# Optimization experiments

Hardware: AMD Instinct MI355X
Metric: run time of the kernel (lower is better)

## Reference

```python
import jax, jax.numpy as jnp
import numpy as np

EPS = 1e-8  # torch.nn.CosineSimilarity default eps

B, N, C, H, W = 256, 5, 640, 10, 10
OC, OH, OW = 32, 5, 5  # AdaptiveAvgPool3d output (input_dim, 5, 5)


def _pool(v):
    # Adaptive avg pool over last 3 dims (C,H,W) -> (OC,OH,OW).
    # Exact block-mean since C%OC==0, H%OH==0, W%OW==0.
    lead = v.shape[:-3]
    v = v.reshape(lead + (OC, C // OC, OH, H // OH, OW, W // OW))
    return v.mean(axis=(-5, -3, -1))


def setup_inputs() -> dict:
    key = jax.random.key(0)
    x = jax.random.normal(key, (B, N, C, H, W), dtype=jnp.float32)
    return {"x": x}


def reference(x) -> jnp.ndarray:
    b, n = x.shape[0], x.shape[1]
    # proxy: pool of the sum over shots -> [B, OC*OH*OW]
    proxy = _pool(x.sum(axis=1)).reshape(b, -1)
    # per-shot pooled features -> [B, N, OC*OH*OW]
    feats = _pool(x).reshape(b, n, -1)
    # cosine similarity (torch formula: dot / max(||a||*||b||, eps))
    dot = jnp.einsum('bnd,bd->bn', feats, proxy)
    na = jnp.linalg.norm(feats, axis=-1)          # [B, N]
    nb = jnp.linalg.norm(proxy, axis=-1)[:, None]  # [B, 1]
    sim = dot / jnp.maximum(na * nb, EPS)          # [B, N]
    # weighted sum of raw shot features -> [B, C, H, W]
    out = jnp.einsum('bn,bnchw->bchw', sim, x)
    return out
```

## Files before the change

kernel.cpp:

```cpp
#include <hip/hip_runtime.h>

#define BB 256
#define NN 5
#define CC_ 640
#define HH 10
#define WW 10
#define CHW 64000
#define DD 800
#define EPSF 1e-8f

__global__ __launch_bounds__(256) void k_pool(const float* __restrict__ x,
                                              float* __restrict__ feats) {
    const int bn = blockIdx.x;
    const float2* __restrict__ xp =
        reinterpret_cast<const float2*>(x + (size_t)bn * CHW);
    float* __restrict__ fp = feats + (size_t)bn * DD;
    for (int d = threadIdx.x; d < DD; d += 256) {
        const int oc  = d / 25;
        const int rem = d - oc * 25;
        const int oh  = rem / 5;
        const int ow  = rem - oh * 5;
        int base = oc * 20 * 50 + oh * 10 + ow;
        float s = 0.f;
        #pragma unroll
        for (int cc = 0; cc < 20; ++cc) {
            float2 a = xp[base + cc * 50];
            float2 b = xp[base + cc * 50 + 5];
            s += (a.x + a.y) + (b.x + b.y);
        }
        fp[d] = s * (1.0f / 80.0f);
    }
}

__global__ __launch_bounds__(64) void k_sim(const float* __restrict__ feats,
                                            float* __restrict__ sim) {
    const int b = blockIdx.x;
    const int lane = threadIdx.x;
    const float* __restrict__ fb = feats + (size_t)b * NN * DD;
    float dot[NN] = {0.f, 0.f, 0.f, 0.f, 0.f};
    float na2[NN] = {0.f, 0.f, 0.f, 0.f, 0.f};
    float nb2 = 0.f;
    for (int d = lane; d < DD; d += 64) {
        float f[NN];
        float p = 0.f;
        #pragma unroll
        for (int n = 0; n < NN; ++n) { f[n] = fb[n * DD + d]; p += f[n]; }
        #pragma unroll
        for (int n = 0; n < NN; ++n) {
            dot[n] += f[n] * p;
            na2[n] += f[n] * f[n];
        }
        nb2 += p * p;
    }
    #pragma unroll
    for (int off = 32; off >= 1; off >>= 1) {
        #pragma unroll
        for (int n = 0; n < NN; ++n) {
            dot[n] += __shfl_down(dot[n], off, 64);
            na2[n] += __shfl_down(na2[n], off, 64);
        }
        nb2 += __shfl_down(nb2, off, 64);
    }
    if (lane == 0) {
        const float nb = sqrtf(nb2);
        #pragma unroll
        for (int n = 0; n < NN; ++n) {
            const float denom = fmaxf(sqrtf(na2[n]) * nb, EPSF);
            sim[b * NN + n] = dot[n] / denom;
        }
    }
}

__global__ __launch_bounds__(256) void k_out(const float* __restrict__ x,
                                             const float* __restrict__ sim,
                                             float* __restrict__ out) {
    const int i = blockIdx.x * 256 + threadIdx.x;
    const int b = i / 16000;
    const int r = i - b * 16000;
    const float4* __restrict__ xp =
        reinterpret_cast<const float4*>(x) + (size_t)b * (NN * 16000) + r;
    const float s0 = sim[b * NN + 0];
    const float s1 = sim[b * NN + 1];
    const float s2 = sim[b * NN + 2];
    const float s3 = sim[b * NN + 3];
    const float s4 = sim[b * NN + 4];
    const float4 a0 = xp[0 * 16000];
    const float4 a1 = xp[1 * 16000];
    const float4 a2 = xp[2 * 16000];
    const float4 a3 = xp[3 * 16000];
    const float4 a4 = xp[4 * 16000];
    float4 o;
    o.x = s0 * a0.x + s1 * a1.x + s2 * a2.x + s3 * a3.x + s4 * a4.x;
    o.y = s0 * a0.y + s1 * a1.y + s2 * a2.y + s3 * a3.y + s4 * a4.y;
    o.z = s0 * a0.z + s1 * a1.z + s2 * a2.z + s3 * a3.z + s4 * a4.z;
    o.w = s0 * a0.w + s1 * a1.w + s2 * a2.w + s3 * a3.w + s4 * a4.w;
    reinterpret_cast<float4*>(out)[i] = o;
}

extern "C" void kernel_launch(void* const* d_in, const int* in_sizes, int n_in,
                              void* d_out, int out_size, void* d_ws, size_t ws_size,
                              hipStream_t stream) {
    const float* x = (const float*)d_in[0];
    float* out = (float*)d_out;
    float* feats = (float*)d_ws;
    float* sim = feats + (size_t)BB * NN * DD;

    k_pool<<<BB * NN, 256, 0, stream>>>(x, feats);
    k_sim<<<BB, 64, 0, stream>>>(feats, sim);
    k_out<<<BB * 16000 / 256, 256, 0, stream>>>(x, sim, out);
}
```

Before: 142.6 us.

## Fuse pool, similarity and weighted sum into one persistent kernel

```diff
diff --git a/kernel.cpp b/kernel.cpp
--- a/kernel.cpp
+++ b/kernel.cpp
@@ -2,99 +2,98 @@
 
 #define BB 256
 #define NN 5
-#define CC_ 640
-#define HH 10
-#define WW 10
 #define CHW 64000
 #define DD 800
 #define EPSF 1e-8f
 
-__global__ __launch_bounds__(256) void k_pool(const float* __restrict__ x,
-                                              float* __restrict__ feats) {
-    const int bn = blockIdx.x;
-    const float2* __restrict__ xp =
-        reinterpret_cast<const float2*>(x + (size_t)bn * CHW);
-    float* __restrict__ fp = feats + (size_t)bn * DD;
-    for (int d = threadIdx.x; d < DD; d += 256) {
-        const int oc  = d / 25;
-        const int rem = d - oc * 25;
-        const int oh  = rem / 5;
-        const int ow  = rem - oh * 5;
-        int base = oc * 20 * 50 + oh * 10 + ow;
-        float s = 0.f;
-        #pragma unroll
-        for (int cc = 0; cc < 20; ++cc) {
-            float2 a = xp[base + cc * 50];
-            float2 b = xp[base + cc * 50 + 5];
-            s += (a.x + a.y) + (b.x + b.y);
+#define NBLOCKS 128
+#define TPB 1024
+
+typedef float f4 __attribute__((ext_vector_type(4)));
+
+__global__ __launch_bounds__(TPB) void k_fused(const float* __restrict__ x,
+                                               float* __restrict__ out) {
+    __shared__ float feats[NN][DD];
+    __shared__ float s_sim[NN];
+    const int tid = threadIdx.x;
+
+    for (int b = blockIdx.x; b < BB; b += gridDim.x) {
+        const float* __restrict__ xb = x + (size_t)b * NN * CHW;
+
+        for (int idx = tid; idx < NN * DD; idx += TPB) {
+            const int n = idx / DD;
+            const int d = idx - n * DD;
+            const int oc  = d / 25;
+            const int rem = d - oc * 25;
+            const int oh  = rem / 5;
+            const int ow  = rem - oh * 5;
+            const float2* __restrict__ xp =
+                reinterpret_cast<const float2*>(xb + (size_t)n * CHW);
+            const int base = oc * 20 * 50 + oh * 10 + ow;
+            float s = 0.f;
+            #pragma unroll
+            for (int cc = 0; cc < 20; ++cc) {
+                float2 a = xp[base + cc * 50];
+                float2 c = xp[base + cc * 50 + 5];
+                s += (a.x + a.y) + (c.x + c.y);
+            }
+            feats[n][d] = s * (1.0f / 80.0f);
         }
-        fp[d] = s * (1.0f / 80.0f);
+        __syncthreads();
+
+        if (tid < 64) {
+            float dot[NN] = {0.f, 0.f, 0.f, 0.f, 0.f};
+            float na2[NN] = {0.f, 0.f, 0.f, 0.f, 0.f};
+            float nb2 = 0.f;
+            for (int d = tid; d < DD; d += 64) {
+                float f[NN];
+                float p = 0.f;
+                #pragma unroll
+                for (int n = 0; n < NN; ++n) { f[n] = feats[n][d]; p += f[n]; }
+                #pragma unroll
+                for (int n = 0; n < NN; ++n) {
+                    dot[n] += f[n] * p;
+                    na2[n] += f[n] * f[n];
+                }
+                nb2 += p * p;
+            }
+            #pragma unroll
+            for (int off = 32; off >= 1; off >>= 1) {
+                #pragma unroll
+                for (int n = 0; n < NN; ++n) {
+                    dot[n] += __shfl_down(dot[n], off, 64);
+                    na2[n] += __shfl_down(na2[n], off, 64);
+                }
+                nb2 += __shfl_down(nb2, off, 64);
+            }
+            if (tid == 0) {
+                const float nb = sqrtf(nb2);
+                #pragma unroll
+                for (int n = 0; n < NN; ++n) {
+                    const float denom = fmaxf(sqrtf(na2[n]) * nb, EPSF);
+                    s_sim[n] = dot[n] / denom;
+                }
+            }
+        }
+        __syncthreads();
+
+        const float s0 = s_sim[0];
+        const float s1 = s_sim[1];
+        const float s2 = s_sim[2];
+        const float s3 = s_sim[3];
+        const float s4 = s_sim[4];
+        const f4* __restrict__ xp4 = reinterpret_cast<const f4*>(xb);
+        f4* __restrict__ op4 = reinterpret_cast<f4*>(out + (size_t)b * CHW);
+        for (int i = tid; i < CHW / 4; i += TPB) {
+            f4 o = s0 * xp4[i]
+                 + s1 * xp4[i + 1 * (CHW / 4)]
+                 + s2 * xp4[i + 2 * (CHW / 4)]
+                 + s3 * xp4[i + 3 * (CHW / 4)]
+                 + s4 * xp4[i + 4 * (CHW / 4)];
+            __builtin_nontemporal_store(o, op4 + i);
+        }
+        __syncthreads();
     }
-}
-
-__global__ __launch_bounds__(64) void k_sim(const float* __restrict__ feats,
-                                            float* __restrict__ sim) {
-    const int b = blockIdx.x;
-    const int lane = threadIdx.x;
-    const float* __restrict__ fb = feats + (size_t)b * NN * DD;
-    float dot[NN] = {0.f, 0.f, 0.f, 0.f, 0.f};
-    float na2[NN] = {0.f, 0.f, 0.f, 0.f, 0.f};
-    float nb2 = 0.f;
-    for (int d = lane; d < DD; d += 64) {
-        float f[NN];
-        float p = 0.f;
-        #pragma unroll
-        for (int n = 0; n < NN; ++n) { f[n] = fb[n * DD + d]; p += f[n]; }
-        #pragma unroll
-        for (int n = 0; n < NN; ++n) {
-            dot[n] += f[n] * p;
-            na2[n] += f[n] * f[n];
-        }
-        nb2 += p * p;
-    }
-    #pragma unroll
-    for (int off = 32; off >= 1; off >>= 1) {
-        #pragma unroll
-        for (int n = 0; n < NN; ++n) {
-            dot[n] += __shfl_down(dot[n], off, 64);
-            na2[n] += __shfl_down(na2[n], off, 64);
-        }
-        nb2 += __shfl_down(nb2, off, 64);
-    }
-    if (lane == 0) {
-        const float nb = sqrtf(nb2);
-        #pragma unroll
-        for (int n = 0; n < NN; ++n) {
-            const float denom = fmaxf(sqrtf(na2[n]) * nb, EPSF);
-            sim[b * NN + n] = dot[n] / denom;
-        }
-    }
-}
-
-__global__ __launch_bounds__(256) void k_out(const float* __restrict__ x,
-                                             const float* __restrict__ sim,
-                                             float* __restrict__ out) {
-    const int i = blockIdx.x * 256 + threadIdx.x;
-    const int b = i / 16000;
-    const int r = i - b * 16000;
-    const float4* __restrict__ xp =
-        reinterpret_cast<const float4*>(x) + (size_t)b * (NN * 16000) + r;
-    const float s0 = sim[b * NN + 0];
-    const float s1 = sim[b * NN + 1];
-    const float s2 = sim[b * NN + 2];
-    const float s3 = sim[b * NN + 3];
-    const float s4 = sim[b * NN + 4];
-    const float4 a0 = xp[0 * 16000];
-    const float4 a1 = xp[1 * 16000];
-    const float4 a2 = xp[2 * 16000];
-    const float4 a3 = xp[3 * 16000];
-    const float4 a4 = xp[4 * 16000];
-    float4 o;
-    o.x = s0 * a0.x + s1 * a1.x + s2 * a2.x + s3 * a3.x + s4 * a4.x;
-    o.y = s0 * a0.y + s1 * a1.y + s2 * a2.y + s3 * a3.y + s4 * a4.y;
-    o.z = s0 * a0.z + s1 * a1.z + s2 * a2.z + s3 * a3.z + s4 * a4.z;
-    o.w = s0 * a0.w + s1 * a1.w + s2 * a2.w + s3 * a3.w + s4 * a4.w;
-    reinterpret_cast<float4*>(out)[i] = o;
 }
 
 extern "C" void kernel_launch(void* const* d_in, const int* in_sizes, int n_in,
@@ -102,10 +101,5 @@
                               hipStream_t stream) {
     const float* x = (const float*)d_in[0];
     float* out = (float*)d_out;
-    float* feats = (float*)d_ws;
-    float* sim = feats + (size_t)BB * NN * DD;
-
-    k_pool<<<BB * NN, 256, 0, stream>>>(x, feats);
-    k_sim<<<BB, 64, 0, stream>>>(feats, sim);
-    k_out<<<BB * 16000 / 256, 256, 0, stream>>>(x, sim, out);
+    k_fused<<<NBLOCKS, TPB, 0, stream>>>(x, out);
 }
```

Result: no change. 141.7 us (-0.6%).
